# Performance work log

Hardware: AMD Instinct MI355X
Metric: run time of the kernel (lower is better)

## Reference

```python
import jax, jax.numpy as jnp
import numpy as np

# Forest layout: 6 levels, children of node i at level L are contiguous at level L+1.
LEVEL_SIZES = [4096, 16384, 65536, 131072, 262144, 262144]
OFF = np.concatenate([[0], np.cumsum(LEVEL_SIZES)]).astype(np.int64)
N_NODES = int(OFF[-1])
VOCAB = 50000
D_IN = 128
HID = 128
N_CLASS = 4
W_SCALE = 0.08  # keep gate pre-activations in a sane range


def setup_inputs() -> dict:
    key = jax.random.key(0)
    ks = jax.random.split(key, 24)
    inp = {}
    inp["sen"] = jax.random.randint(ks[0], (N_NODES,), 0, VOCAB, dtype=jnp.int32)
    inp["embedding"] = jax.random.normal(ks[1], (VOCAB, D_IN), jnp.float32)
    names = ["ix", "ih", "fx", "fh", "ox", "oh", "ux", "uh"]
    for j, nm in enumerate(names):
        din = D_IN if nm.endswith("x") else HID
        inp["W_" + nm] = jax.random.normal(ks[2 + j], (din, HID), jnp.float32) * W_SCALE
        inp["b_" + nm] = jnp.zeros((HID,), jnp.float32)
    inp["W_out"] = jax.random.normal(ks[20], (HID, N_CLASS), jnp.float32) * W_SCALE
    inp["b_out"] = jnp.zeros((N_CLASS,), jnp.float32)
    return inp


def _forward(sen, embedding, W_ix, b_ix, W_ih, b_ih, W_fx, b_fx, W_fh, b_fh,
             W_ox, b_ox, W_oh, b_oh, W_ux, b_ux, W_uh, b_uh, W_out, b_out):
    emb = embedding[sen]                               # [N, D_in] gather
    h_all = jnp.zeros((N_NODES, HID), emb.dtype)
    c_all = jnp.zeros((N_NODES, HID), emb.dtype)
    L_last = len(LEVEL_SIZES) - 1
    for L in range(L_last, -1, -1):                    # bottom-up over levels
        o0, o1 = int(OFF[L]), int(OFF[L + 1])
        nL = LEVEL_SIZES[L]
        x = emb[o0:o1]                                 # [nL, D_in]
        if L == L_last:                                # leaves: no children
            h_sum = jnp.zeros((nL, HID), emb.dtype)
            fc_sum = jnp.zeros((nL, HID), emb.dtype)
        else:
            c0, c1 = int(OFF[L + 1]), int(OFF[L + 2])
            ratio = LEVEL_SIZES[L + 1] // nL           # children per node
            hc = h_all[c0:c1].reshape(nL, ratio, HID)  # children h
            cc = c_all[c0:c1].reshape(nL, ratio, HID)  # children c
            h_sum = hc.sum(axis=1)
            # per-child forget gate: sigmoid(fx(x_parent) + fh(h_child))
            f = jax.nn.sigmoid((x @ W_fx + b_fx)[:, None, :] + hc @ W_fh + b_fh)
            fc_sum = (f * cc).sum(axis=1)
        i = jax.nn.sigmoid(x @ W_ix + b_ix + h_sum @ W_ih + b_ih)
        og = jax.nn.sigmoid(x @ W_ox + b_ox + h_sum @ W_oh + b_oh)
        u = jnp.tanh(x @ W_ux + b_ux + h_sum @ W_uh + b_uh)
        c = i * u + fc_sum
        h = og * jnp.tanh(c)
        h_all = h_all.at[o0:o1].set(h)
        c_all = c_all.at[o0:o1].set(c)
    root_h = h_all[: LEVEL_SIZES[0]]                   # level-0 nodes
    return root_h @ W_out + b_out                      # [n_roots, 4] logits


def reference(sen, embedding, W_ix, b_ix, W_ih, b_ih, W_fx, b_fx, W_fh, b_fh,
              W_ox, b_ox, W_oh, b_oh, W_ux, b_ux, W_uh, b_uh, W_out, b_out):
    return _forward(sen, embedding, W_ix, b_ix, W_ih, b_ih, W_fx, b_fx, W_fh, b_fh,
                    W_ox, b_ox, W_oh, b_oh, W_ux, b_ux, W_uh, b_uh, W_out, b_out)
```

## Files before the change

kernel.cpp:

```cpp
#include <hip/hip_runtime.h>
#include <hip/hip_bf16.h>
#include <cstdio>

typedef unsigned short u16;
typedef __bf16 bf16x8 __attribute__((ext_vector_type(8)));
typedef float  floatx4 __attribute__((ext_vector_type(4)));

__device__ __forceinline__ float bf2f(u16 u) {
  union { unsigned int i; float f; } v; v.i = ((unsigned int)u) << 16; return v.f;
}
__device__ __forceinline__ u16 f2bf(float f) {
  union { float f; unsigned int i; } v; v.f = f;
  unsigned int x = v.i;
  return (u16)((x + 0x7fffu + ((x >> 16) & 1u)) >> 16);
}
__device__ __forceinline__ unsigned int f2bf_pk(float a, float b) {
  __hip_bfloat162 h = __float22bfloat162_rn(make_float2(a, b));
  union { __hip_bfloat162 h; unsigned int u; } v; v.h = h; return v.u;
}
__device__ __forceinline__ float sigmoidf_(float x) {
  return __builtin_amdgcn_rcpf(1.f + __expf(-x));
}
__device__ __forceinline__ float tanhf_(float x) {
  return fmaf(-2.f, __builtin_amdgcn_rcpf(1.f + __expf(2.f * x)), 1.f);
}

__device__ __forceinline__ int swz128(int row, int c16) {
  return row * 128 + ((c16 ^ (row & 15)) << 3);
}
__device__ __forceinline__ int swze(int row, int col) {
  return row * 128 + (((((col >> 3)) ^ (row & 15)) << 3) | (col & 7));
}

__global__ __launch_bounds__(256, 2) void proj_e(
    const float* __restrict__ emb, const u16* __restrict__ WT,
    const float* __restrict__ bsum, u16* __restrict__ Ep)
{
  __shared__ __align__(16) u16 ldsA[128 * 128];
  const int tid = threadIdx.x;
  const long m0 = (long)blockIdx.x * 128;
  {
    const int r = tid >> 1, half = tid & 1;
    long row = m0 + r; if (row > 49999) row = 49999;
    const float* src = emb + row * 128 + half * 64;
#pragma unroll
    for (int i = 0; i < 8; i++) {
      float4 v0 = *reinterpret_cast<const float4*>(src + i * 8);
      float4 v1 = *reinterpret_cast<const float4*>(src + i * 8 + 4);
      unsigned int ov[4] = { f2bf_pk(v0.x, v0.y), f2bf_pk(v0.z, v0.w),
                             f2bf_pk(v1.x, v1.y), f2bf_pk(v1.z, v1.w) };
      *reinterpret_cast<uint4*>(&ldsA[swz128(r, half * 8 + i)]) =
          *reinterpret_cast<const uint4*>(ov);
    }
  }
  __syncthreads();
  const int lane = tid & 63, w = tid >> 6, l16 = lane & 15, quad = lane >> 4;
#pragma unroll
  for (int half = 0; half < 2; half++) {
    const int col = w * 32 + half * 16 + l16;
    bf16x8 bI[4], bU[4], bO[4], bF[4];
#pragma unroll
    for (int ks = 0; ks < 4; ks++) {
      const size_t o_ = ks * 32 + quad * 8;
      bI[ks] = *reinterpret_cast<const bf16x8*>(WT + (size_t)(0   + col) * 128 + o_);
      bU[ks] = *reinterpret_cast<const bf16x8*>(WT + (size_t)(128 + col) * 128 + o_);
      bO[ks] = *reinterpret_cast<const bf16x8*>(WT + (size_t)(256 + col) * 128 + o_);
      bF[ks] = *reinterpret_cast<const bf16x8*>(WT + (size_t)(384 + col) * 128 + o_);
    }
    const float bi = bsum[col], bu = bsum[128 + col], bo = bsum[256 + col], bf = bsum[384 + col];
#pragma unroll
    for (int i = 0; i < 8; i++) {
      floatx4 aI = {0.f,0.f,0.f,0.f}, aU = {0.f,0.f,0.f,0.f};
      floatx4 aO = {0.f,0.f,0.f,0.f}, aF = {0.f,0.f,0.f,0.f};
#pragma unroll
      for (int ks = 0; ks < 4; ks++) {
        bf16x8 a = *reinterpret_cast<const bf16x8*>(&ldsA[swz128(i * 16 + l16, ks * 4 + quad)]);
        aI = __builtin_amdgcn_mfma_f32_16x16x32_bf16(a, bI[ks], aI, 0, 0, 0);
        aU = __builtin_amdgcn_mfma_f32_16x16x32_bf16(a, bU[ks], aU, 0, 0, 0);
        aO = __builtin_amdgcn_mfma_f32_16x16x32_bf16(a, bO[ks], aO, 0, 0, 0);
        aF = __builtin_amdgcn_mfma_f32_16x16x32_bf16(a, bF[ks], aF, 0, 0, 0);
      }
#pragma unroll
      for (int r2 = 0; r2 < 4; r2++) {
        const long row = m0 + i * 16 + quad * 4 + r2;
        if (row < 50000) {
          u16 ov[4] = { f2bf(aI[r2] + bi), f2bf(aU[r2] + bu),
                        f2bf(aO[r2] + bo), f2bf(aF[r2] + bf) };
          *reinterpret_cast<ushort4*>(Ep + row * 512 + col * 4) =
              *reinterpret_cast<const ushort4*>(ov);
        }
      }
    }
  }
}

__global__ __launch_bounds__(256, 2) void proj_hc(
    const u16* __restrict__ Ep,
    const u16* __restrict__ BihT, const u16* __restrict__ BuhT,
    const u16* __restrict__ BohT, const u16* __restrict__ BfT,
    u16* __restrict__ Cl, u16* __restrict__ Gh)
{
  __shared__ __align__(16) u16 ldsA[128 * 128];
  const int tid = threadIdx.x;
  const long m0 = (long)blockIdx.x * 128;
  {
    const int r = tid >> 1, half = tid & 1;
    long row = m0 + r;
    const bool ok = (row < 50000); if (!ok) row = 49999;
    const u16* src = Ep + row * 512 + half * 256;
#pragma unroll
    for (int i = 0; i < 8; i++) {
      uint4 v[4];
#pragma unroll
      for (int k = 0; k < 4; k++)
        v[k] = *reinterpret_cast<const uint4*>(src + i * 32 + k * 8);
      unsigned int hp[4], cp[4];
#pragma unroll
      for (int k = 0; k < 4; k++) {
        const u16* p = reinterpret_cast<const u16*>(&v[k]);
        float c0 = sigmoidf_(bf2f(p[0])) * tanhf_(bf2f(p[1]));
        float c1 = sigmoidf_(bf2f(p[4])) * tanhf_(bf2f(p[5]));
        float h0 = sigmoidf_(bf2f(p[2])) * tanhf_(c0);
        float h1 = sigmoidf_(bf2f(p[6])) * tanhf_(c1);
        cp[k] = f2bf_pk(c0, c1);
        hp[k] = f2bf_pk(h0, h1);
      }
      *reinterpret_cast<uint4*>(&ldsA[swz128(r, half * 8 + i)]) =
          *reinterpret_cast<const uint4*>(hp);
      if (ok)
        *reinterpret_cast<uint4*>(Cl + row * 128 + half * 64 + i * 8) =
            *reinterpret_cast<const uint4*>(cp);
    }
  }
  __syncthreads();
  const int lane = tid & 63, w = tid >> 6, l16 = lane & 15, quad = lane >> 4;
#pragma unroll
  for (int half = 0; half < 2; half++) {
    const int col = w * 32 + half * 16 + l16;
    bf16x8 bI[4], bU[4], bO[4], bF[4];
#pragma unroll
    for (int ks = 0; ks < 4; ks++) {
      const size_t o_ = (size_t)col * 128 + ks * 32 + quad * 8;
      bI[ks] = *reinterpret_cast<const bf16x8*>(BihT + o_);
      bU[ks] = *reinterpret_cast<const bf16x8*>(BuhT + o_);
      bO[ks] = *reinterpret_cast<const bf16x8*>(BohT + o_);
      bF[ks] = *reinterpret_cast<const bf16x8*>(BfT  + o_);
    }
#pragma unroll
    for (int i = 0; i < 8; i++) {
      floatx4 aI = {0.f,0.f,0.f,0.f}, aU = {0.f,0.f,0.f,0.f};
      floatx4 aO = {0.f,0.f,0.f,0.f}, aF = {0.f,0.f,0.f,0.f};
#pragma unroll
      for (int ks = 0; ks < 4; ks++) {
        bf16x8 a = *reinterpret_cast<const bf16x8*>(&ldsA[swz128(i * 16 + l16, ks * 4 + quad)]);
        aI = __builtin_amdgcn_mfma_f32_16x16x32_bf16(a, bI[ks], aI, 0, 0, 0);
        aU = __builtin_amdgcn_mfma_f32_16x16x32_bf16(a, bU[ks], aU, 0, 0, 0);
        aO = __builtin_amdgcn_mfma_f32_16x16x32_bf16(a, bO[ks], aO, 0, 0, 0);
        aF = __builtin_amdgcn_mfma_f32_16x16x32_bf16(a, bF[ks], aF, 0, 0, 0);
      }
#pragma unroll
      for (int r2 = 0; r2 < 4; r2++) {
        const long row = m0 + i * 16 + quad * 4 + r2;
        if (row < 50000) {
          u16 ov[4] = { f2bf(aI[r2]), f2bf(aU[r2]), f2bf(aO[r2]), f2bf(aF[r2]) };
          *reinterpret_cast<ushort4*>(Gh + row * 512 + col * 4) =
              *reinterpret_cast<const ushort4*>(ov);
        }
      }
    }
  }
}

__global__ __launch_bounds__(256) void l4_leaf(
    const int* __restrict__ sen, const u16* __restrict__ Ep,
    const u16* __restrict__ Gh, const u16* __restrict__ Cl,
    u16* __restrict__ c_out, u16* __restrict__ h_out,
    long o0, long co0)
{
  const int lane = threadIdx.x & 63, w = threadIdx.x >> 6;
  const long p = (long)blockIdx.x * 4 + w;
  const size_t vp = (size_t)sen[o0 + p];
  const size_t vc = (size_t)sen[co0 + p];
  uint4 e = *reinterpret_cast<const uint4*>(Ep + vp * 512 + (size_t)lane * 8);
  uint4 g = *reinterpret_cast<const uint4*>(Gh + vc * 512 + (size_t)lane * 8);
  unsigned int cl2 = *reinterpret_cast<const unsigned int*>(Cl + vc * 128 + (size_t)lane * 2);
  const u16* ep = reinterpret_cast<const u16*>(&e);
  const u16* gp = reinterpret_cast<const u16*>(&g);
  const float cl0 = bf2f((u16)(cl2 & 0xffffu)), cl1 = bf2f((u16)(cl2 >> 16));
  const float i0 = sigmoidf_(bf2f(ep[0]) + bf2f(gp[0]));
  const float u0 = tanhf_   (bf2f(ep[1]) + bf2f(gp[1]));
  const float o0g= sigmoidf_(bf2f(ep[2]) + bf2f(gp[2]));
  const float f0 = sigmoidf_(bf2f(ep[3]) + bf2f(gp[3]));
  const float i1 = sigmoidf_(bf2f(ep[4]) + bf2f(gp[4]));
  const float u1 = tanhf_   (bf2f(ep[5]) + bf2f(gp[5]));
  const float o1g= sigmoidf_(bf2f(ep[6]) + bf2f(gp[6]));
  const float f1 = sigmoidf_(bf2f(ep[7]) + bf2f(gp[7]));
  const float c0 = fmaf(i0, u0, f0 * cl0);
  const float c1 = fmaf(i1, u1, f1 * cl1);
  const float h0 = o0g * tanhf_(c0);
  const float h1 = o1g * tanhf_(c1);
  *reinterpret_cast<unsigned int*>(c_out + p * 128 + lane * 2) = f2bf_pk(c0, c1);
  *reinterpret_cast<unsigned int*>(h_out + p * 128 + lane * 2) = f2bf_pk(h0, h1);
}

template<int LR, bool LEAF>
__global__ __launch_bounds__(256, 2) void k_level(
    const int* __restrict__ sen, const u16* __restrict__ Ep,
    const u16* __restrict__ h_prev, const u16* __restrict__ c_prev,
    const u16* __restrict__ BfT, const u16* __restrict__ BihT,
    const u16* __restrict__ BuhT, const u16* __restrict__ BohT,
    u16* __restrict__ c_out, u16* __restrict__ h_out,
    long o0, long co0)
{
  constexpr int PM  = (LR == 2) ? 32 : 64;
  constexpr int CM  = PM << LR;
  constexpr int NCI = CM / 16;
  constexpr int RT  = 1 << LR;
  constexpr int RTI = 4 >> LR;
  constexpr int TPR = 256 / CM;
  __shared__ __align__(16) u16 ldsA[CM * 128];
  __shared__ __align__(16) u16 ldsC[LEAF ? CM * 128 : 8];
  __shared__ int sidP[PM];

  const int tid = threadIdx.x;
  const long p0 = (long)blockIdx.x * PM;
  const long cb = (long)blockIdx.x * CM;

  {
    const int r = tid / TPR, q = tid % TPR;
    constexpr int CH = 16 / TPR;
    if (LEAF) {
      const size_t v = (size_t)sen[co0 + cb + r];
      const u16* hs = h_prev + v * 128;
      const u16* cs = c_prev + v * 128;
#pragma unroll
      for (int ii = 0; ii < CH; ii++) {
        const int c16 = q * CH + ii;
        *reinterpret_cast<uint4*>(&ldsA[swz128(r, c16)]) =
            *reinterpret_cast<const uint4*>(hs + c16 * 8);
        *reinterpret_cast<uint4*>(&ldsC[swz128(r, c16)]) =
            *reinterpret_cast<const uint4*>(cs + c16 * 8);
      }
    } else {
      const u16* src = h_prev + (cb + r) * 128;
#pragma unroll
      for (int ii = 0; ii < CH; ii++) {
        const int c16 = q * CH + ii;
        *reinterpret_cast<uint4*>(&ldsA[swz128(r, c16)]) =
            *reinterpret_cast<const uint4*>(src + c16 * 8);
      }
    }
    if (tid < PM) sidP[tid] = sen[o0 + p0 + tid];
  }
  __syncthreads();

  const int lane = tid & 63, w = tid >> 6, l16 = lane & 15, quad = lane >> 4;

#pragma unroll
  for (int gl = 0; gl < 2; gl++) {
    const int col = w * 32 + gl * 16 + l16;
    bf16x8 bF[4], bI[4], bU[4], bO[4];
#pragma unroll
    for (int ks = 0; ks < 4; ks++) {
      const size_t bo_ = (size_t)col * 128 + ks * 32 + quad * 8;
      bF[ks] = *reinterpret_cast<const bf16x8*>(BfT + bo_);
      bI[ks] = *reinterpret_cast<const bf16x8*>(BihT + bo_);
      bU[ks] = *reinterpret_cast<const bf16x8*>(BuhT + bo_);
      bO[ks] = *reinterpret_cast<const bf16x8*>(BohT + bo_);
    }
#pragma unroll
    for (int i = 0; i < NCI; i++) {
      floatx4 aF = {0.f,0.f,0.f,0.f}, aI = {0.f,0.f,0.f,0.f};
      floatx4 aU = {0.f,0.f,0.f,0.f}, aO = {0.f,0.f,0.f,0.f};
#pragma unroll
      for (int ks = 0; ks < 4; ks++) {
        bf16x8 a = *reinterpret_cast<const bf16x8*>(&ldsA[swz128(i * 16 + l16, ks * 4 + quad)]);
        aF = __builtin_amdgcn_mfma_f32_16x16x32_bf16(a, bF[ks], aF, 0, 0, 0);
        aI = __builtin_amdgcn_mfma_f32_16x16x32_bf16(a, bI[ks], aI, 0, 0, 0);
        aU = __builtin_amdgcn_mfma_f32_16x16x32_bf16(a, bU[ks], aU, 0, 0, 0);
        aO = __builtin_amdgcn_mfma_f32_16x16x32_bf16(a, bO[ks], aO, 0, 0, 0);
      }
      const int rbase = i * 16 + quad * 4;
#pragma unroll
      for (int t = 0; t < RTI; t++) {
        const int p = (rbase >> LR) + t;
        ushort4 g4 = *reinterpret_cast<const ushort4*>(Ep + (size_t)sidP[p] * 512 + col * 4);
        const float epf = bf2f(g4.w);
        float fsum = 0.f, isum = 0.f, usum = 0.f, osum = 0.f;
#pragma unroll
        for (int r2 = t * RT; r2 < t * RT + RT; r2++) {
          const int row = rbase + r2;
          const float cch = LEAF ? bf2f(ldsC[swze(row, col)])
                                 : bf2f(c_prev[(cb + row) * 128 + col]);
          fsum += sigmoidf_(aF[r2] + epf) * cch;
          isum += aI[r2]; usum += aU[r2]; osum += aO[r2];
        }
        const float c = sigmoidf_(isum + bf2f(g4.x)) * tanhf_(usum + bf2f(g4.y)) + fsum;
        const float h = sigmoidf_(osum + bf2f(g4.z)) * tanhf_(c);
        c_out[(p0 + p) * 128 + col] = f2bf(c);
        h_out[(p0 + p) * 128 + col] = f2bf(h);
      }
    }
  }
}

__global__ void build_wallT(const float* __restrict__ Wix, const float* __restrict__ Wux,
                            const float* __restrict__ Wox, const float* __restrict__ Wfx,
                            u16* __restrict__ WT)
{
  int idx = blockIdx.x * 256 + threadIdx.x;
  int n = idx >> 7, k = idx & 127;
  int g = n >> 7, j = n & 127;
  const float* W = (g == 0) ? Wix : (g == 1) ? Wux : (g == 2) ? Wox : Wfx;
  WT[idx] = f2bf(W[k * 128 + j]);
}

__global__ void build_bsum(const float* __restrict__ b_ix, const float* __restrict__ b_ih,
                           const float* __restrict__ b_ux, const float* __restrict__ b_uh,
                           const float* __restrict__ b_ox, const float* __restrict__ b_oh,
                           const float* __restrict__ b_fx, const float* __restrict__ b_fh,
                           float* __restrict__ bsum)
{
  int n = blockIdx.x * 256 + threadIdx.x;
  int g = n >> 7, j = n & 127;
  float v = (g == 0) ? b_ix[j] + b_ih[j] : (g == 1) ? b_ux[j] + b_uh[j]
          : (g == 2) ? b_ox[j] + b_oh[j] : b_fx[j] + b_fh[j];
  bsum[n] = v;
}

__global__ void build_bt128(const float* __restrict__ W, u16* __restrict__ BT) {
  int idx = blockIdx.x * 256 + threadIdx.x;
  int n = idx >> 7, k = idx & 127;
  BT[idx] = f2bf(W[k * 128 + n]);
}

__global__ void out_proj(const u16* __restrict__ h_root, const float* __restrict__ W_out,
                         const float* __restrict__ b_out, float* __restrict__ out)
{
  int idx = blockIdx.x * 256 + threadIdx.x;
  int n = idx >> 2, cls = idx & 3;
  float s = b_out[cls];
  for (int k = 0; k < 128; k++)
    s += bf2f(h_root[(long)n * 128 + k]) * W_out[k * 4 + cls];
  out[idx] = s;
}

extern "C" void kernel_launch(void* const* d_in, const int* in_sizes, int n_in,
                              void* d_out, int out_size, void* d_ws, size_t ws_size,
                              hipStream_t stream)
{
  const int*   sen  = (const int*)d_in[0];
  const float* emb  = (const float*)d_in[1];
  const float* W_ix = (const float*)d_in[2];  const float* b_ix = (const float*)d_in[3];
  const float* W_ih = (const float*)d_in[4];  const float* b_ih = (const float*)d_in[5];
  const float* W_fx = (const float*)d_in[6];  const float* b_fx = (const float*)d_in[7];
  const float* W_fh = (const float*)d_in[8];  const float* b_fh = (const float*)d_in[9];
  const float* W_ox = (const float*)d_in[10]; const float* b_ox = (const float*)d_in[11];
  const float* W_oh = (const float*)d_in[12]; const float* b_oh = (const float*)d_in[13];
  const float* W_ux = (const float*)d_in[14]; const float* b_ux = (const float*)d_in[15];
  const float* W_uh = (const float*)d_in[16]; const float* b_uh = (const float*)d_in[17];
  const float* W_out= (const float*)d_in[18]; const float* b_out= (const float*)d_in[19];
  float* out = (float*)d_out;

  const size_t AH  = (size_t)262144 * 128;
  const size_t BH  = (size_t)131072 * 128;
  const size_t EPB = (size_t)50000 * 512 * 2;
  const size_t CLB = (size_t)50000 * 128 * 2;
  const size_t SCR = 2 * BH * 2;
  const size_t need = 2 * AH * 2 + SCR + EPB
                    + (size_t)512 * 128 * 2 + 4 * (size_t)128 * 128 * 2 + 512 * 4 + 4096;
  fprintf(stderr, "[tree_lstm] ws_size=%zu need=%zu\n", ws_size, need);
  if (ws_size < need) {
    fprintf(stderr, "[tree_lstm] INSUFFICIENT WORKSPACE — skipping launch\n");
    return;
  }
  char* ws = (char*)d_ws;
  size_t off = 0;
  auto take = [&](size_t bytes) { char* p = ws + off; off += (bytes + 255) & ~(size_t)255; return p; };
  u16* hA = (u16*)take(AH * 2);
  u16* cA = (u16*)take(AH * 2);
  char* S  = take(SCR);
  u16* Ep = (u16*)take(EPB);
  u16* WallT = (u16*)take((size_t)512 * 128 * 2);
  u16* BihT = (u16*)take((size_t)128 * 128 * 2);
  u16* BuhT = (u16*)take((size_t)128 * 128 * 2);
  u16* BohT = (u16*)take((size_t)128 * 128 * 2);
  u16* BfhT = (u16*)take((size_t)128 * 128 * 2);
  float* bsum = (float*)take(512 * 4);

  u16* Cl = (u16*)S;
  u16* Gh = (u16*)(S + CLB);
  u16* hB = (u16*)S;
  u16* cB = (u16*)(S + BH * 2);

  build_wallT<<<256, 256, 0, stream>>>(W_ix, W_ux, W_ox, W_fx, WallT);
  build_bsum<<<2, 256, 0, stream>>>(b_ix, b_ih, b_ux, b_uh, b_ox, b_oh, b_fx, b_fh, bsum);
  build_bt128<<<64, 256, 0, stream>>>(W_ih, BihT);
  build_bt128<<<64, 256, 0, stream>>>(W_uh, BuhT);
  build_bt128<<<64, 256, 0, stream>>>(W_oh, BohT);
  build_bt128<<<64, 256, 0, stream>>>(W_fh, BfhT);
  proj_e<<<391, 256, 0, stream>>>(emb, WallT, bsum, Ep);
  proj_hc<<<391, 256, 0, stream>>>(Ep, BihT, BuhT, BohT, BfhT, Cl, Gh);

  const long LOFF[6] = {0, 4096, 20480, 86016, 217088, 479232};

  l4_leaf<<<65536, 256, 0, stream>>>(sen, Ep, Gh, Cl, cA, hA, LOFF[4], LOFF[5]);
  k_level<1, false><<<2048, 256, 0, stream>>>(sen, Ep, hA, cA,
      BfhT, BihT, BuhT, BohT, cB, hB, LOFF[3], 0);
  k_level<1, false><<<1024, 256, 0, stream>>>(sen, Ep, hB, cB,
      BfhT, BihT, BuhT, BohT, cA, hA, LOFF[2], 0);
  k_level<2, false><<<512, 256, 0, stream>>>(sen, Ep, hA, cA,
      BfhT, BihT, BuhT, BohT, cB, hB, LOFF[1], 0);
  k_level<2, false><<<128, 256, 0, stream>>>(sen, Ep, hB, cB,
      BfhT, BihT, BuhT, BohT, cA, hA, LOFF[0], 0);

  out_proj<<<64, 256, 0, stream>>>(hA, W_out, b_out, out);
}
```

Measured before the change: 541.5 us.

## Fuse level-4 node computation into level-3 kernel via shared memory

Replaces the standalone level-4 kernel and the separate level-3 launch with one fused kernel. Each block computes the h and c values of its level-4 children from the precomputed projection tables, writes them into shared memory, and then runs the level-3 MFMA step on them directly. This removes the global-memory write and re-read of the 262144-node level-4 state plus one kernel launch. Workspace is also re-laid out with per-level buffers instead of aliasing scratch regions. The fused kernel does more per-thread elementwise work and uses more shared memory, which may lower occupancy.

```diff
diff --git a/kernel.cpp b/kernel.cpp
--- a/kernel.cpp
+++ b/kernel.cpp
@@ -171,46 +171,126 @@
   }
 }
 
-__global__ __launch_bounds__(256) void l4_leaf(
+__global__ __launch_bounds__(256, 2) void k_l3fused(
     const int* __restrict__ sen, const u16* __restrict__ Ep,
     const u16* __restrict__ Gh, const u16* __restrict__ Cl,
+    const u16* __restrict__ BfT, const u16* __restrict__ BihT,
+    const u16* __restrict__ BuhT, const u16* __restrict__ BohT,
     u16* __restrict__ c_out, u16* __restrict__ h_out,
-    long o0, long co0)
-{
-  const int lane = threadIdx.x & 63, w = threadIdx.x >> 6;
-  const long p = (long)blockIdx.x * 4 + w;
-  const size_t vp = (size_t)sen[o0 + p];
-  const size_t vc = (size_t)sen[co0 + p];
-  uint4 e = *reinterpret_cast<const uint4*>(Ep + vp * 512 + (size_t)lane * 8);
-  uint4 g = *reinterpret_cast<const uint4*>(Gh + vc * 512 + (size_t)lane * 8);
-  unsigned int cl2 = *reinterpret_cast<const unsigned int*>(Cl + vc * 128 + (size_t)lane * 2);
-  const u16* ep = reinterpret_cast<const u16*>(&e);
-  const u16* gp = reinterpret_cast<const u16*>(&g);
-  const float cl0 = bf2f((u16)(cl2 & 0xffffu)), cl1 = bf2f((u16)(cl2 >> 16));
-  const float i0 = sigmoidf_(bf2f(ep[0]) + bf2f(gp[0]));
-  const float u0 = tanhf_   (bf2f(ep[1]) + bf2f(gp[1]));
-  const float o0g= sigmoidf_(bf2f(ep[2]) + bf2f(gp[2]));
-  const float f0 = sigmoidf_(bf2f(ep[3]) + bf2f(gp[3]));
-  const float i1 = sigmoidf_(bf2f(ep[4]) + bf2f(gp[4]));
-  const float u1 = tanhf_   (bf2f(ep[5]) + bf2f(gp[5]));
-  const float o1g= sigmoidf_(bf2f(ep[6]) + bf2f(gp[6]));
-  const float f1 = sigmoidf_(bf2f(ep[7]) + bf2f(gp[7]));
-  const float c0 = fmaf(i0, u0, f0 * cl0);
-  const float c1 = fmaf(i1, u1, f1 * cl1);
-  const float h0 = o0g * tanhf_(c0);
-  const float h1 = o1g * tanhf_(c1);
-  *reinterpret_cast<unsigned int*>(c_out + p * 128 + lane * 2) = f2bf_pk(c0, c1);
-  *reinterpret_cast<unsigned int*>(h_out + p * 128 + lane * 2) = f2bf_pk(h0, h1);
-}
-
-template<int LR, bool LEAF>
+    long o0, long o1, long o2)
+{
+  constexpr int PM = 64, CM = 128, NCI = 8, RT = 2;
+  __shared__ __align__(16) u16 ldsA[CM * 128];
+  __shared__ __align__(16) u16 ldsC[CM * 128];
+  __shared__ int sidP[PM];
+
+  const int tid = threadIdx.x;
+  const long p0 = (long)blockIdx.x * PM;
+  const long cb = (long)blockIdx.x * CM;
+
+  {
+    const int r = tid >> 1, q = tid & 1;
+    const size_t vp = (size_t)sen[o1 + cb + r];
+    const size_t vc = (size_t)sen[o2 + cb + r];
+    const u16* ep = Ep + vp * 512 + q * 256;
+    const u16* gh = Gh + vc * 512 + q * 256;
+    const u16* cl = Cl + vc * 128 + q * 64;
+#pragma unroll
+    for (int ii = 0; ii < 8; ii++) {
+      uint4 ev[4], gv[4];
+#pragma unroll
+      for (int k = 0; k < 4; k++) {
+        ev[k] = *reinterpret_cast<const uint4*>(ep + ii * 32 + k * 8);
+        gv[k] = *reinterpret_cast<const uint4*>(gh + ii * 32 + k * 8);
+      }
+      uint4 cvv = *reinterpret_cast<const uint4*>(cl + ii * 8);
+      const u16* cp = reinterpret_cast<const u16*>(&cvv);
+      unsigned int hp[4], cpk[4];
+#pragma unroll
+      for (int k = 0; k < 4; k++) {
+        const u16* e = reinterpret_cast<const u16*>(&ev[k]);
+        const u16* g = reinterpret_cast<const u16*>(&gv[k]);
+        const float i0 = sigmoidf_(bf2f(e[0]) + bf2f(g[0]));
+        const float u0 = tanhf_   (bf2f(e[1]) + bf2f(g[1]));
+        const float og0= sigmoidf_(bf2f(e[2]) + bf2f(g[2]));
+        const float f0 = sigmoidf_(bf2f(e[3]) + bf2f(g[3]));
+        const float i1 = sigmoidf_(bf2f(e[4]) + bf2f(g[4]));
+        const float u1 = tanhf_   (bf2f(e[5]) + bf2f(g[5]));
+        const float og1= sigmoidf_(bf2f(e[6]) + bf2f(g[6]));
+        const float f1 = sigmoidf_(bf2f(e[7]) + bf2f(g[7]));
+        const float c0 = fmaf(i0, u0, f0 * bf2f(cp[k * 2]));
+        const float c1 = fmaf(i1, u1, f1 * bf2f(cp[k * 2 + 1]));
+        const float h0 = og0 * tanhf_(c0);
+        const float h1 = og1 * tanhf_(c1);
+        hp[k]  = f2bf_pk(h0, h1);
+        cpk[k] = f2bf_pk(c0, c1);
+      }
+      *reinterpret_cast<uint4*>(&ldsA[swz128(r, q * 8 + ii)]) =
+          *reinterpret_cast<const uint4*>(hp);
+      *reinterpret_cast<uint4*>(&ldsC[swz128(r, q * 8 + ii)]) =
+          *reinterpret_cast<const uint4*>(cpk);
+    }
+    if (tid < PM) sidP[tid] = sen[o0 + p0 + tid];
+  }
+  __syncthreads();
+
+  const int lane = tid & 63, w = tid >> 6, l16 = lane & 15, quad = lane >> 4;
+
+#pragma unroll
+  for (int gl = 0; gl < 2; gl++) {
+    const int col = w * 32 + gl * 16 + l16;
+    bf16x8 bF[4], bI[4], bU[4], bO[4];
+#pragma unroll
+    for (int ks = 0; ks < 4; ks++) {
+      const size_t bo_ = (size_t)col * 128 + ks * 32 + quad * 8;
+      bF[ks] = *reinterpret_cast<const bf16x8*>(BfT + bo_);
+      bI[ks] = *reinterpret_cast<const bf16x8*>(BihT + bo_);
+      bU[ks] = *reinterpret_cast<const bf16x8*>(BuhT + bo_);
+      bO[ks] = *reinterpret_cast<const bf16x8*>(BohT + bo_);
+    }
+#pragma unroll
+    for (int i = 0; i < NCI; i++) {
+      floatx4 aF = {0.f,0.f,0.f,0.f}, aI = {0.f,0.f,0.f,0.f};
+      floatx4 aU = {0.f,0.f,0.f,0.f}, aO = {0.f,0.f,0.f,0.f};
+#pragma unroll
+      for (int ks = 0; ks < 4; ks++) {
+        bf16x8 a = *reinterpret_cast<const bf16x8*>(&ldsA[swz128(i * 16 + l16, ks * 4 + quad)]);
+        aF = __builtin_amdgcn_mfma_f32_16x16x32_bf16(a, bF[ks], aF, 0, 0, 0);
+        aI = __builtin_amdgcn_mfma_f32_16x16x32_bf16(a, bI[ks], aI, 0, 0, 0);
+        aU = __builtin_amdgcn_mfma_f32_16x16x32_bf16(a, bU[ks], aU, 0, 0, 0);
+        aO = __builtin_amdgcn_mfma_f32_16x16x32_bf16(a, bO[ks], aO, 0, 0, 0);
+      }
+      const int rbase = i * 16 + quad * 4;
+#pragma unroll
+      for (int t = 0; t < 2; t++) {
+        const int p = (rbase >> 1) + t;
+        ushort4 g4 = *reinterpret_cast<const ushort4*>(Ep + (size_t)sidP[p] * 512 + col * 4);
+        const float epf = bf2f(g4.w);
+        float fsum = 0.f, isum = 0.f, usum = 0.f, osum = 0.f;
+#pragma unroll
+        for (int r2 = t * RT; r2 < t * RT + RT; r2++) {
+          const int row = rbase + r2;
+          const float cch = bf2f(ldsC[swze(row, col)]);
+          fsum += sigmoidf_(aF[r2] + epf) * cch;
+          isum += aI[r2]; usum += aU[r2]; osum += aO[r2];
+        }
+        const float c = sigmoidf_(isum + bf2f(g4.x)) * tanhf_(usum + bf2f(g4.y)) + fsum;
+        const float h = sigmoidf_(osum + bf2f(g4.z)) * tanhf_(c);
+        c_out[(p0 + p) * 128 + col] = f2bf(c);
+        h_out[(p0 + p) * 128 + col] = f2bf(h);
+      }
+    }
+  }
+}
+
+template<int LR>
 __global__ __launch_bounds__(256, 2) void k_level(
     const int* __restrict__ sen, const u16* __restrict__ Ep,
     const u16* __restrict__ h_prev, const u16* __restrict__ c_prev,
     const u16* __restrict__ BfT, const u16* __restrict__ BihT,
     const u16* __restrict__ BuhT, const u16* __restrict__ BohT,
     u16* __restrict__ c_out, u16* __restrict__ h_out,
-    long o0, long co0)
+    long o0)
 {
   constexpr int PM  = (LR == 2) ? 32 : 64;
   constexpr int CM  = PM << LR;
@@ -219,7 +299,6 @@
   constexpr int RTI = 4 >> LR;
   constexpr int TPR = 256 / CM;
   __shared__ __align__(16) u16 ldsA[CM * 128];
-  __shared__ __align__(16) u16 ldsC[LEAF ? CM * 128 : 8];
   __shared__ int sidP[PM];
 
   const int tid = threadIdx.x;
@@ -229,26 +308,12 @@
   {
     const int r = tid / TPR, q = tid % TPR;
     constexpr int CH = 16 / TPR;
-    if (LEAF) {
-      const size_t v = (size_t)sen[co0 + cb + r];
-      const u16* hs = h_prev + v * 128;
-      const u16* cs = c_prev + v * 128;
-#pragma unroll
-      for (int ii = 0; ii < CH; ii++) {
-        const int c16 = q * CH + ii;
-        *reinterpret_cast<uint4*>(&ldsA[swz128(r, c16)]) =
-            *reinterpret_cast<const uint4*>(hs + c16 * 8);
-        *reinterpret_cast<uint4*>(&ldsC[swz128(r, c16)]) =
-            *reinterpret_cast<const uint4*>(cs + c16 * 8);
-      }
-    } else {
-      const u16* src = h_prev + (cb + r) * 128;
-#pragma unroll
-      for (int ii = 0; ii < CH; ii++) {
-        const int c16 = q * CH + ii;
-        *reinterpret_cast<uint4*>(&ldsA[swz128(r, c16)]) =
-            *reinterpret_cast<const uint4*>(src + c16 * 8);
-      }
+    const u16* src = h_prev + (cb + r) * 128;
+#pragma unroll
+    for (int ii = 0; ii < CH; ii++) {
+      const int c16 = q * CH + ii;
+      *reinterpret_cast<uint4*>(&ldsA[swz128(r, c16)]) =
+          *reinterpret_cast<const uint4*>(src + c16 * 8);
     }
     if (tid < PM) sidP[tid] = sen[o0 + p0 + tid];
   }
@@ -290,8 +355,7 @@
 #pragma unroll
         for (int r2 = t * RT; r2 < t * RT + RT; r2++) {
           const int row = rbase + r2;
-          const float cch = LEAF ? bf2f(ldsC[swze(row, col)])
-                                 : bf2f(c_prev[(cb + row) * 128 + col]);
+          const float cch = bf2f(c_prev[(cb + row) * 128 + col]);
           fsum += sigmoidf_(aF[r2] + epf) * cch;
           isum += aI[r2]; usum += aU[r2]; osum += aO[r2];
         }
@@ -362,13 +426,14 @@
   const float* W_out= (const float*)d_in[18]; const float* b_out= (const float*)d_in[19];
   float* out = (float*)d_out;
 
-  const size_t AH  = (size_t)262144 * 128;
-  const size_t BH  = (size_t)131072 * 128;
   const size_t EPB = (size_t)50000 * 512 * 2;
   const size_t CLB = (size_t)50000 * 128 * 2;
-  const size_t SCR = 2 * BH * 2;
-  const size_t need = 2 * AH * 2 + SCR + EPB
-                    + (size_t)512 * 128 * 2 + 4 * (size_t)128 * 128 * 2 + 512 * 4 + 4096;
+  const size_t H3  = (size_t)131072 * 128 * 2;
+  const size_t H2  = (size_t)65536  * 128 * 2;
+  const size_t H1  = (size_t)16384  * 128 * 2;
+  const size_t H0  = (size_t)4096   * 128 * 2;
+  const size_t need = 2 * EPB + CLB + 2 * (H3 + H2 + H1 + H0)
+                    + (size_t)512 * 128 * 2 + 4 * (size_t)128 * 128 * 2 + 512 * 4 + 8192;
   fprintf(stderr, "[tree_lstm] ws_size=%zu need=%zu\n", ws_size, need);
   if (ws_size < need) {
     fprintf(stderr, "[tree_lstm] INSUFFICIENT WORKSPACE — skipping launch\n");
@@ -377,21 +442,19 @@
   char* ws = (char*)d_ws;
   size_t off = 0;
   auto take = [&](size_t bytes) { char* p = ws + off; off += (bytes + 255) & ~(size_t)255; return p; };
-  u16* hA = (u16*)take(AH * 2);
-  u16* cA = (u16*)take(AH * 2);
-  char* S  = take(SCR);
   u16* Ep = (u16*)take(EPB);
+  u16* Gh = (u16*)take(EPB);
+  u16* Cl = (u16*)take(CLB);
+  u16* h3 = (u16*)take(H3);  u16* c3 = (u16*)take(H3);
+  u16* h2 = (u16*)take(H2);  u16* c2 = (u16*)take(H2);
+  u16* h1 = (u16*)take(H1);  u16* c1 = (u16*)take(H1);
+  u16* h0 = (u16*)take(H0);  u16* c0 = (u16*)take(H0);
   u16* WallT = (u16*)take((size_t)512 * 128 * 2);
   u16* BihT = (u16*)take((size_t)128 * 128 * 2);
   u16* BuhT = (u16*)take((size_t)128 * 128 * 2);
   u16* BohT = (u16*)take((size_t)128 * 128 * 2);
   u16* BfhT = (u16*)take((size_t)128 * 128 * 2);
   float* bsum = (float*)take(512 * 4);
-
-  u16* Cl = (u16*)S;
-  u16* Gh = (u16*)(S + CLB);
-  u16* hB = (u16*)S;
-  u16* cB = (u16*)(S + BH * 2);
 
   build_wallT<<<256, 256, 0, stream>>>(W_ix, W_ux, W_ox, W_fx, WallT);
   build_bsum<<<2, 256, 0, stream>>>(b_ix, b_ih, b_ux, b_uh, b_ox, b_oh, b_fx, b_fh, bsum);
@@ -404,15 +467,14 @@
 
   const long LOFF[6] = {0, 4096, 20480, 86016, 217088, 479232};
 
-  l4_leaf<<<65536, 256, 0, stream>>>(sen, Ep, Gh, Cl, cA, hA, LOFF[4], LOFF[5]);
-  k_level<1, false><<<2048, 256, 0, stream>>>(sen, Ep, hA, cA,
-      BfhT, BihT, BuhT, BohT, cB, hB, LOFF[3], 0);
-  k_level<1, false><<<1024, 256, 0, stream>>>(sen, Ep, hB, cB,
-      BfhT, BihT, BuhT, BohT, cA, hA, LOFF[2], 0);
-  k_level<2, false><<<512, 256, 0, stream>>>(sen, Ep, hA, cA,
-      BfhT, BihT, BuhT, BohT, cB, hB, LOFF[1], 0);
-  k_level<2, false><<<128, 256, 0, stream>>>(sen, Ep, hB, cB,
-      BfhT, BihT, BuhT, BohT, cA, hA, LOFF[0], 0);
-
-  out_proj<<<64, 256, 0, stream>>>(hA, W_out, b_out, out);
-}
+  k_l3fused<<<2048, 256, 0, stream>>>(sen, Ep, Gh, Cl,
+      BfhT, BihT, BuhT, BohT, c3, h3, LOFF[3], LOFF[4], LOFF[5]);
+  k_level<1><<<1024, 256, 0, stream>>>(sen, Ep, h3, c3,
+      BfhT, BihT, BuhT, BohT, c2, h2, LOFF[2]);
+  k_level<2><<<512, 256, 0, stream>>>(sen, Ep, h2, c2,
+      BfhT, BihT, BuhT, BohT, c1, h1, LOFF[1]);
+  k_level<2><<<128, 256, 0, stream>>>(sen, Ep, h1, c1,
+      BfhT, BihT, BuhT, BohT, c0, h0, LOFF[0]);
+
+  out_proj<<<64, 256, 0, stream>>>(h0, W_out, b_out, out);
+}
```

Result: faster. 520.3 us (-3.9%).
